# Performance work log

Hardware: AMD Instinct MI355X
Metric: run time of the kernel (lower is better)

Reference implementation:

```python
import jax, jax.numpy as jnp
import numpy as np

N_NODES = 50000
N_EDGES = 600000
NODE_IN = 32
EDGE_IN = 16
HID = 128
L = 3
GCTX = 64


def _lin_init(key, out_d, in_d):
    kw, kb = jax.random.split(key)
    bound = 1.0 / np.sqrt(in_d)
    w = jax.random.uniform(kw, (out_d, in_d), minval=-bound, maxval=bound, dtype=jnp.float32)
    b = jax.random.uniform(kb, (out_d,), minval=-bound, maxval=bound, dtype=jnp.float32)
    return w, b


def _stack_lin(key, out_d, in_d, n):
    ws, bs = [], []
    for k in jax.random.split(key, n):
        w, b = _lin_init(k, out_d, in_d)
        ws.append(w); bs.append(b)
    return jnp.stack(ws), jnp.stack(bs)


def setup_inputs() -> dict:
    key = jax.random.key(0)
    ks = jax.random.split(key, 16)
    x = jax.random.normal(ks[0], (N_NODES, NODE_IN), dtype=jnp.float32)
    edge_index = jax.random.randint(ks[1], (2, N_EDGES), 0, N_NODES, dtype=jnp.int64)
    edge_attr = jax.random.normal(ks[2], (N_EDGES, EDGE_IN), dtype=jnp.float32)
    global_context = jax.random.normal(ks[3], (GCTX,), dtype=jnp.float32)
    node_proj_w, node_proj_b = _lin_init(ks[4], HID, NODE_IN)
    msg_w1, msg_b1 = _stack_lin(ks[5], HID, HID + EDGE_IN, L)
    msg_w2, msg_b2 = _stack_lin(ks[6], HID, HID, L)
    attn_w1, attn_b1 = _stack_lin(ks[7], HID // 2, 2 * HID + EDGE_IN, L)
    attn_w2, attn_b2 = _stack_lin(ks[8], 1, HID // 2, L)
    upd_w1, upd_b1 = _stack_lin(ks[9], HID, 2 * HID, L)
    upd_w2, upd_b2 = _stack_lin(ks[10], HID, HID, L)
    ln_g = jnp.ones((L, HID), dtype=jnp.float32)
    ln_b = jnp.zeros((L, HID), dtype=jnp.float32)
    q_w1, q_b1 = _lin_init(ks[11], HID, HID + GCTX)
    q_w2, q_b2 = _lin_init(ks[12], 1, HID)
    return {
        "x": x, "edge_index": edge_index, "edge_attr": edge_attr,
        "global_context": global_context,
        "node_proj_w": node_proj_w, "node_proj_b": node_proj_b,
        "msg_w1": msg_w1, "msg_b1": msg_b1, "msg_w2": msg_w2, "msg_b2": msg_b2,
        "attn_w1": attn_w1, "attn_b1": attn_b1, "attn_w2": attn_w2, "attn_b2": attn_b2,
        "upd_w1": upd_w1, "upd_b1": upd_b1, "upd_w2": upd_w2, "upd_b2": upd_b2,
        "ln_g": ln_g, "ln_b": ln_b,
        "q_w1": q_w1, "q_b1": q_b1, "q_w2": q_w2, "q_b2": q_b2,
    }


def _layernorm(x, g, b, eps=1e-5):
    mu = jnp.mean(x, axis=-1, keepdims=True)
    var = jnp.var(x, axis=-1, keepdims=True)
    return (x - mu) * jax.lax.rsqrt(var + eps) * g + b


def _mp_layer(h, src, dst, ea, p):
    hs = h[src]          # [E, HID] gather
    hd = h[dst]          # [E, HID] gather
    # message MLP
    m = jnp.concatenate([hs, ea], axis=1)
    m = jax.nn.relu(m @ p["mw1"].T + p["mb1"])
    msg = m @ p["mw2"].T + p["mb2"]
    # attention scores
    a = jnp.concatenate([hs, hd, ea], axis=1)
    a = jax.nn.leaky_relu(a @ p["aw1"].T + p["ab1"], negative_slope=0.2)
    scores = (a @ p["aw2"].T + p["ab2"])[:, 0]  # [E]
    exp_scores = jnp.exp(scores - jnp.max(scores))  # global max, as in original
    sum_exp = jnp.zeros((h.shape[0],), dtype=h.dtype).at[dst].add(exp_scores)
    weights = exp_scores / (sum_exp[dst] + 1e-6)
    agg = jnp.zeros_like(h).at[dst].add(msg * weights[:, None])
    # update MLP + residual + layernorm
    u = jnp.concatenate([h, agg], axis=1)
    u = jax.nn.relu(u @ p["uw1"].T + p["ub1"])
    out = u @ p["uw2"].T + p["ub2"]
    return _layernorm(jax.nn.relu(out + h), p["g"], p["b"])


def reference(x, edge_index, edge_attr, global_context,
              node_proj_w, node_proj_b,
              msg_w1, msg_b1, msg_w2, msg_b2,
              attn_w1, attn_b1, attn_w2, attn_b2,
              upd_w1, upd_b1, upd_w2, upd_b2,
              ln_g, ln_b, q_w1, q_b1, q_w2, q_b2):
    src, dst = edge_index[0], edge_index[1]
    h = jax.nn.relu(x @ node_proj_w.T + node_proj_b)
    for i in range(L):
        p = {"mw1": msg_w1[i], "mb1": msg_b1[i], "mw2": msg_w2[i], "mb2": msg_b2[i],
             "aw1": attn_w1[i], "ab1": attn_b1[i], "aw2": attn_w2[i], "ab2": attn_b2[i],
             "uw1": upd_w1[i], "ub1": upd_b1[i], "uw2": upd_w2[i], "ub2": upd_b2[i],
             "g": ln_g[i], "b": ln_b[i]}
        h = _mp_layer(h, src, dst, edge_attr, p)
    ctx = jnp.broadcast_to(global_context[None, :], (h.shape[0], GCTX))
    h = jnp.concatenate([h, ctx], axis=1)
    q = jax.nn.relu(h @ q_w1.T + q_b1) @ q_w2.T + q_b2
    return q[:, 0]
```

## Files before the change

### kernel.cpp

```cpp
#include <hip/hip_runtime.h>
#include <hip/hip_bf16.h>

#define N_NODES 50000
#define N_EDGES 600000
#define NODE_IN 32
#define EDGE_IN 16
#define HID 128
#define NLAYER 3
#define GCTX 64

typedef _Float16 h2 __attribute__((ext_vector_type(2)));
typedef _Float16 f16x8 __attribute__((ext_vector_type(8)));
typedef float f32x4 __attribute__((ext_vector_type(4)));

__device__ __forceinline__ float bf2f(unsigned short u) {
  union { unsigned int i; float f; } c; c.i = ((unsigned int)u) << 16; return c.f;
}
__device__ __forceinline__ unsigned int bfp2hp(unsigned int b) {
  union { unsigned int i; float f; } lo, hi;
  lo.i = b << 16; hi.i = b & 0xffff0000u;
  h2 r; r.x = (_Float16)lo.f; r.y = (_Float16)hi.f;
  union { h2 h; unsigned int u; } c; c.h = r; return c.u;
}
__device__ __forceinline__ h2 u2h2(unsigned int u) {
  union { unsigned int u; h2 h; } c; c.u = u; return c.h;
}
__device__ __forceinline__ float dot2(h2 a, h2 b, float c) {
#if __has_builtin(__builtin_amdgcn_fdot2)
  return __builtin_amdgcn_fdot2(a, b, c, false);
#else
  return c + (float)a.x * (float)b.x + (float)a.y * (float)b.y;
#endif
}

__device__ __forceinline__ unsigned int load_pair(const void* p, size_t pairIdx, int fm) {
  if (fm == 0) return bfp2hp(((const unsigned int*)p)[pairIdx]);
  if (fm == 2) return ((const unsigned int*)p)[pairIdx];
  const float* f = (const float*)p;
  h2 r; r.x = (_Float16)f[2 * pairIdx]; r.y = (_Float16)f[2 * pairIdx + 1];
  union { h2 h; unsigned int u; } c; c.h = r; return c.u;
}
__device__ __forceinline__ float load_scal(const void* p, size_t idx, int fm) {
  if (fm == 0) return bf2f(((const unsigned short*)p)[idx]);
  if (fm == 2) return (float)((const _Float16*)p)[idx];
  return ((const float*)p)[idx];
}
__device__ __forceinline__ int load_idx(const void* p, size_t pos, int im) {
  if (im == 0) return ((const int*)p)[pos];
  return (int)((const long long*)p)[pos];
}
__device__ __forceinline__ uint4 zero4() { uint4 z; z.x = z.y = z.z = z.w = 0u; return z; }
__device__ __forceinline__ uint4 load8(const void* p, size_t eoff, int fm) {
  uint4 r;
  if (fm == 0) {
    uint4 t = *(const uint4*)((const unsigned short*)p + eoff);
    r.x = bfp2hp(t.x); r.y = bfp2hp(t.y); r.z = bfp2hp(t.z); r.w = bfp2hp(t.w);
  } else if (fm == 2) {
    r = *(const uint4*)((const unsigned short*)p + eoff);
  } else {
    const float* f = (const float*)p + eoff;
    h2 a, b, c, d;
    a.x = (_Float16)f[0]; a.y = (_Float16)f[1];
    b.x = (_Float16)f[2]; b.y = (_Float16)f[3];
    c.x = (_Float16)f[4]; c.y = (_Float16)f[5];
    d.x = (_Float16)f[6]; d.y = (_Float16)f[7];
    union { h2 h; unsigned int u; } ua, ub, uc, ud;
    ua.h = a; ub.h = b; uc.h = c; ud.h = d;
    r.x = ua.u; r.y = ub.u; r.z = uc.u; r.w = ud.u;
  }
  return r;
}
__device__ __forceinline__ f32x4 mfma16(uint4 a, uint4 b, f32x4 c) {
  union { uint4 u; f16x8 h; } A, B; A.u = a; B.u = b;
  return __builtin_amdgcn_mfma_f32_16x16x32_f16(A.h, B.h, c, 0, 0, 0);
}

__device__ __forceinline__ float wave_sum(float v) {
  for (int m = 32; m >= 1; m >>= 1) v += __shfl_xor(v, m, 64);
  return v;
}
__device__ __forceinline__ float wave_max(float v) {
  for (int m = 32; m >= 1; m >>= 1) v = fmaxf(v, __shfl_xor(v, m, 64));
  return v;
}

__global__ __launch_bounds__(256) void k_detect(const unsigned int* __restrict__ x,
                                                const unsigned int* __restrict__ ei,
                                                int* __restrict__ flags) {
  __shared__ int sIn, sOddNZ;
  const int tid = threadIdx.x;
  if (tid == 0) { sIn = 0; sOddNZ = 0; }
  __syncthreads();
  int cnt = 0;
  for (int i = tid; i < 2048; i += 256) {
    unsigned int d = x[i];
    float v0 = fabsf(bf2f((unsigned short)(d & 0xffff)));
    float v1 = fabsf(bf2f((unsigned short)(d >> 16)));
    if (v0 >= 0.1f && v0 <= 6.0f) cnt++;
    if (v1 >= 0.1f && v1 <= 6.0f) cnt++;
  }
  int nz = 0;
  for (int i = tid; i < 512; i += 256)
    if (ei[2 * i + 1] != 0) nz++;
  atomicAdd(&sIn, cnt);
  atomicAdd(&sOddNZ, nz);
  __syncthreads();
  if (tid == 0) {
    float frac = (float)sIn / 4096.f;
    flags[0] = (frac > 0.75f) ? 0 : ((frac >= 0.3f) ? 1 : 2);
    flags[1] = (sOddNZ < 4) ? 1 : 0;
  }
}

__global__ __launch_bounds__(256) void k_proj(
    const void* __restrict__ x, const void* __restrict__ W,
    const void* __restrict__ b, _Float16* __restrict__ h,
    const int* __restrict__ flags) {
  const int fm = flags[0];
  const int tid = threadIdx.x;
  const int slot = tid >> 7;
  const int t = tid & 127;
  __shared__ __align__(16) _Float16 sX[2][NODE_IN];
  unsigned int w[16];
#pragma unroll
  for (int i = 0; i < 16; ++i) w[i] = load_pair(W, (size_t)t * 16 + i, fm);
  const float bias = load_scal(b, t, fm);
  unsigned int* sx32 = (unsigned int*)sX[slot];
  for (int base = blockIdx.x * 2; base < N_NODES; base += gridDim.x * 2) {
    const int n = base + slot;
    if (t < 16) sx32[t] = load_pair(x, (size_t)n * 16 + t, fm);
    __syncthreads();
    float a0 = bias, a1 = 0.f, a2 = 0.f, a3 = 0.f;
    const uint4* vq = (const uint4*)sx32;
#pragma unroll
    for (int q = 0; q < 4; ++q) {
      uint4 v = vq[q];
      a0 = dot2(u2h2(v.x), u2h2(w[q * 4 + 0]), a0);
      a1 = dot2(u2h2(v.y), u2h2(w[q * 4 + 1]), a1);
      a2 = dot2(u2h2(v.z), u2h2(w[q * 4 + 2]), a2);
      a3 = dot2(u2h2(v.w), u2h2(w[q * 4 + 3]), a3);
    }
    h[(size_t)n * HID + t] = (_Float16)fmaxf((a0 + a1) + (a2 + a3), 0.f);
    __syncthreads();
  }
}

__global__ __launch_bounds__(256) void k_hist(const void* __restrict__ ei,
                                              int* __restrict__ cnt,
                                              const int* __restrict__ flags) {
  const int im = flags[1];
  for (int e = blockIdx.x * 256 + threadIdx.x; e < N_EDGES; e += gridDim.x * 256)
    atomicAdd(&cnt[load_idx(ei, N_EDGES + e, im)], 1);
}
__global__ __launch_bounds__(256) void k_scan(const int* __restrict__ cnt,
                                              int* __restrict__ row_ptr,
                                              int* __restrict__ cur) {
  __shared__ int sPart[256];
  const int t = threadIdx.x;
  const int c0 = t * 196;
  const int c1 = (c0 + 196 < N_NODES) ? c0 + 196 : N_NODES;
  int s = 0;
  for (int i = c0; i < c1; ++i) s += cnt[i];
  sPart[t] = s;
  __syncthreads();
  if (t == 0) {
    int run = 0;
    for (int i = 0; i < 256; ++i) { int v = sPart[i]; sPart[i] = run; run += v; }
    row_ptr[N_NODES] = run;
  }
  __syncthreads();
  int off = sPart[t];
  for (int i = c0; i < c1; ++i) {
    row_ptr[i] = off; cur[i] = off; off += cnt[i];
  }
}
__global__ __launch_bounds__(256) void k_scatter(const void* __restrict__ ei,
                                                 const void* __restrict__ ea,
                                                 int* __restrict__ cur,
                                                 int2* __restrict__ sd2,
                                                 _Float16* __restrict__ eaPerm,
                                                 const int* __restrict__ flags) {
  const int im = flags[1], fm = flags[0];
  for (int e = blockIdx.x * 256 + threadIdx.x; e < N_EDGES; e += gridDim.x * 256) {
    const int s = load_idx(ei, e, im);
    const int d = load_idx(ei, N_EDGES + e, im);
    const int pos = atomicAdd(&cur[d], 1);
    int2 sd; sd.x = s; sd.y = d;
    sd2[pos] = sd;
    uint4 lo = load8(ea, (size_t)e * 16, fm);
    uint4 hi = load8(ea, (size_t)e * 16 + 8, fm);
    *(uint4*)(eaPerm + (size_t)pos * 16) = lo;
    *(uint4*)(eaPerm + (size_t)pos * 16 + 8) = hi;
  }
}

#define SAP 296
#define SM1P 136
#define NT32 (N_EDGES / 32)

__global__ __launch_bounds__(256) void k_edge(
    const _Float16* __restrict__ h, const int2* __restrict__ sd2,
    const _Float16* __restrict__ eaPerm,
    const void* __restrict__ aw1, const void* __restrict__ ab1,
    const void* __restrict__ aw2, const void* __restrict__ ab2,
    const void* __restrict__ mw1, const void* __restrict__ mb1,
    float* __restrict__ scores, float* __restrict__ pmax,
    _Float16* __restrict__ msgbuf, const int* __restrict__ flags, int lay) {
  const int fm = flags[0];
  const int tid = threadIdx.x;
  const int w = tid >> 6, l = tid & 63;
  const int m16 = l & 15, q = l >> 4;
  __shared__ __align__(16) _Float16 sA[2][32 * SAP];
  __shared__ float sS[2][4][32];

  uint4 bA[9], bM1[2][5];
  {
    const int arow = w * 16 + m16;
    const size_t awb = (size_t)lay * 64 * 272 + (size_t)arow * 272;
#pragma unroll
    for (int ks = 0; ks < 9; ++ks) {
      const int c0 = ks * 32 + q * 8;
      bA[ks] = (c0 < 272) ? load8(aw1, awb + c0, fm) : zero4();
    }
#pragma unroll
    for (int nt = 0; nt < 2; ++nt) {
      const int mrow = (2 * w + nt) * 16 + m16;
      const size_t m1b = (size_t)lay * 128 * 144 + (size_t)mrow * 144;
#pragma unroll
      for (int ks = 0; ks < 5; ++ks) {
        const int c0 = ks * 32 + q * 8;
        bM1[nt][ks] = (c0 < 144) ? load8(mw1, m1b + c0, fm) : zero4();
      }
    }
  }
  const float ab1v = load_scal(ab1, lay * 64 + w * 16 + m16, fm);
  const float w2s  = load_scal(aw2, lay * 64 + w * 16 + m16, fm);
  const float b2f  = load_scal(ab2, lay, fm);
  float b1v[2];
#pragma unroll
  for (int nt = 0; nt < 2; ++nt)
    b1v[nt] = load_scal(mb1, lay * 128 + (2 * w + nt) * 16 + m16, fm);

  const int ide0 = tid >> 4, ch = tid & 15, ide1 = ide0 + 16;
  float lmax = -3.4e38f;
  uint4 rHs0, rHd0, rHs1, rHd1, rEa;
  const int G = gridDim.x;
  int t = blockIdx.x, pt = -1, buf = 0;

  if (tid < 128) {
    const int b = tid >> 6, s = tid & 63;
    *(uint4*)(sA[b] + (s >> 1) * SAP + 272 + (s & 1) * 8) = zero4();
  }
  {
    const int e0 = t * 32;
    const int2 s0 = sd2[e0 + ide0], s1 = sd2[e0 + ide1];
    rHs0 = *(const uint4*)(h + (size_t)s0.x * HID + ch * 8);
    rHd0 = *(const uint4*)(h + (size_t)s0.y * HID + ch * 8);
    rHs1 = *(const uint4*)(h + (size_t)s1.x * HID + ch * 8);
    rHd1 = *(const uint4*)(h + (size_t)s1.y * HID + ch * 8);
    if (tid < 64)
      rEa = *(const uint4*)(eaPerm + (size_t)(e0 + (tid >> 1)) * 16 + (tid & 1) * 8);
  }
  __syncthreads();

  while (t < NT32) {
    _Float16* A = sA[buf];
    *(uint4*)(A + ide0 * SAP + ch * 8) = rHs0;
    *(uint4*)(A + ide0 * SAP + 128 + ch * 8) = rHd0;
    *(uint4*)(A + ide1 * SAP + ch * 8) = rHs1;
    *(uint4*)(A + ide1 * SAP + 128 + ch * 8) = rHd1;
    if (tid < 64)
      *(uint4*)(A + (tid >> 1) * SAP + 256 + (tid & 1) * 8) = rEa;
    __syncthreads();
    const int nxt = t + G;
    if (nxt < NT32) {
      const int e0 = nxt * 32;
      const int2 s0 = sd2[e0 + ide0], s1 = sd2[e0 + ide1];
      rHs0 = *(const uint4*)(h + (size_t)s0.x * HID + ch * 8);
      rHd0 = *(const uint4*)(h + (size_t)s0.y * HID + ch * 8);
      rHs1 = *(const uint4*)(h + (size_t)s1.x * HID + ch * 8);
      rHd1 = *(const uint4*)(h + (size_t)s1.y * HID + ch * 8);
      if (tid < 64)
        rEa = *(const uint4*)(eaPerm + (size_t)(e0 + (tid >> 1)) * 16 + (tid & 1) * 8);
    }
#pragma unroll
    for (int mg = 0; mg < 2; ++mg) {
      const int arow = m16 + 16 * mg;
      uint4 aF[9];
#pragma unroll
      for (int ks = 0; ks < 9; ++ks)
        aF[ks] = *(const uint4*)(A + arow * SAP + ks * 32 + q * 8);
      {
        f32x4 aacc = {0.f, 0.f, 0.f, 0.f};
#pragma unroll
        for (int ks = 0; ks < 9; ++ks) aacc = mfma16(aF[ks], bA[ks], aacc);
        float sv[4];
#pragma unroll
        for (int r = 0; r < 4; ++r) {
          float v = aacc[r] + ab1v;
          v = (v > 0.f) ? v : 0.2f * v;
          sv[r] = v * w2s;
        }
#pragma unroll
        for (int mk = 1; mk <= 8; mk <<= 1) {
#pragma unroll
          for (int r = 0; r < 4; ++r) sv[r] += __shfl_xor(sv[r], mk, 64);
        }
        if (m16 == 0)
          *(float4*)(&sS[buf][w][mg * 16 + q * 4]) = make_float4(sv[0], sv[1], sv[2], sv[3]);
      }
#pragma unroll
      for (int nt = 0; nt < 2; ++nt) {
        f32x4 macc = {0.f, 0.f, 0.f, 0.f};
#pragma unroll
        for (int ks = 0; ks < 4; ++ks) macc = mfma16(aF[ks], bM1[nt][ks], macc);
        macc = mfma16(aF[8], bM1[nt][4], macc);
        const int col = (2 * w + nt) * 16 + m16;
#pragma unroll
        for (int r = 0; r < 4; ++r)
          msgbuf[(size_t)(t * 32 + mg * 16 + q * 4 + r) * HID + col] =
              (_Float16)fmaxf(macc[r] + b1v[nt], 0.f);
      }
    }
    if (pt >= 0 && tid < 32) {
      const float s = sS[buf ^ 1][0][tid] + sS[buf ^ 1][1][tid] +
                      sS[buf ^ 1][2][tid] + sS[buf ^ 1][3][tid] + b2f;
      scores[pt * 32 + tid] = s;
      lmax = fmaxf(lmax, s);
    }
    pt = t; t = nxt; buf ^= 1;
  }
  __syncthreads();
  if (pt >= 0 && tid < 32) {
    const float s = sS[buf ^ 1][0][tid] + sS[buf ^ 1][1][tid] +
                    sS[buf ^ 1][2][tid] + sS[buf ^ 1][3][tid] + b2f;
    scores[pt * 32 + tid] = s;
    lmax = fmaxf(lmax, s);
  }
  if (w == 0) {
    float m = wave_max((l < 32) ? lmax : -3.4e38f);
    if (tid == 0) pmax[blockIdx.x] = m;
  }
}

__global__ __launch_bounds__(256) void k_rmax(const float* __restrict__ pmax, int n,
                                              float* __restrict__ gmax) {
  float m = -3.4e38f;
  for (int i = threadIdx.x; i < n; i += 256) m = fmaxf(m, pmax[i]);
  m = wave_max(m);
  __shared__ float sm[4];
  if ((threadIdx.x & 63) == 0) sm[threadIdx.x >> 6] = m;
  __syncthreads();
  if (threadIdx.x == 0) gmax[0] = fmaxf(fmaxf(sm[0], sm[1]), fmaxf(sm[2], sm[3]));
}

__global__ __launch_bounds__(256) void k_gather(
    const _Float16* __restrict__ msgbuf, const float* __restrict__ scores,
    const int* __restrict__ row_ptr, const float* __restrict__ gmax,
    _Float16* __restrict__ Sbuf, float* __restrict__ Dbuf) {
  const int w = threadIdx.x >> 6, l = threadIdx.x & 63;
  const int n0 = blockIdx.x * 16;
  const float M = gmax[0];
  const unsigned int* mb32 = (const unsigned int*)msgbuf;
#pragma unroll
  for (int k = 0; k < 4; ++k) {
    const int n = n0 + 4 * w + k;
    const int rp0 = row_ptr[n], rp1 = row_ptr[n + 1];
    float ax0 = 0.f, ay0 = 0.f, d0s = 0.f;
    float ax1 = 0.f, ay1 = 0.f, d1s = 0.f;
    float ax2 = 0.f, ay2 = 0.f, d2s = 0.f;
    float ax3 = 0.f, ay3 = 0.f, d3s = 0.f;
    int i = rp0;
    for (; i + 4 <= rp1; i += 4) {
      const float s0 = scores[i], s1 = scores[i + 1];
      const float s2 = scores[i + 2], s3 = scores[i + 3];
      const unsigned int m0 = mb32[(size_t)i * 64 + l];
      const unsigned int m1 = mb32[(size_t)(i + 1) * 64 + l];
      const unsigned int m2 = mb32[(size_t)(i + 2) * 64 + l];
      const unsigned int m3 = mb32[(size_t)(i + 3) * 64 + l];
      const float w0 = __expf(s0 - M), w1 = __expf(s1 - M);
      const float w2 = __expf(s2 - M), w3 = __expf(s3 - M);
      h2 p0 = u2h2(m0), p1 = u2h2(m1), p2 = u2h2(m2), p3 = u2h2(m3);
      ax0 += w0 * (float)p0.x; ay0 += w0 * (float)p0.y; d0s += w0;
      ax1 += w1 * (float)p1.x; ay1 += w1 * (float)p1.y; d1s += w1;
      ax2 += w2 * (float)p2.x; ay2 += w2 * (float)p2.y; d2s += w2;
      ax3 += w3 * (float)p3.x; ay3 += w3 * (float)p3.y; d3s += w3;
    }
    for (; i < rp1; ++i) {
      const float w0 = __expf(scores[i] - M);
      h2 p0 = u2h2(mb32[(size_t)i * 64 + l]);
      ax0 += w0 * (float)p0.x; ay0 += w0 * (float)p0.y; d0s += w0;
    }
    const float ax = (ax0 + ax1) + (ax2 + ax3);
    const float ay = (ay0 + ay1) + (ay2 + ay3);
    const float den = (d0s + d1s) + (d2s + d3s);
    h2 o; o.x = (_Float16)ax; o.y = (_Float16)ay;
    union { h2 hh; unsigned int u; } c; c.hh = o;
    ((unsigned int*)Sbuf)[(size_t)n * 64 + l] = c.u;
    if (l == 0) Dbuf[n] = den;
  }
}

#define SUP3 392
#define SOP 132
__global__ __launch_bounds__(256, 1) void k_upd3(
    _Float16* __restrict__ h, const _Float16* __restrict__ Sbuf,
    const float* __restrict__ Dbuf,
    const void* __restrict__ mw2, const void* __restrict__ mb2,
    const void* __restrict__ uw1, const void* __restrict__ ub1,
    const void* __restrict__ uw2, const void* __restrict__ ub2,
    const void* __restrict__ lng, const void* __restrict__ lnb,
    const int* __restrict__ flags, int lay) {
  const int fm = flags[0];
  const int tid = threadIdx.x;
  const int w = tid >> 6, l = tid & 63;
  const int m16 = l & 15, q = l >> 4;
  __shared__ __align__(16) _Float16 sU[16 * SUP3];
  __shared__ __align__(16) _Float16 sM1[16 * SM1P];
  __shared__ __align__(16) float sO[16 * SOP];
  __shared__ float sD[16];

  uint4 bU1[2][8], bU2[2][4], bM2g[2][4];
  float b1v[2], b2v[2], b2m[2];
#pragma unroll
  for (int nt = 0; nt < 2; ++nt) {
    const int row = w * 32 + nt * 16 + m16;
    const size_t b1p = (size_t)lay * 128 * 256 + (size_t)row * 256;
#pragma unroll
    for (int ks = 0; ks < 8; ++ks) bU1[nt][ks] = load8(uw1, b1p + ks * 32 + q * 8, fm);
    const size_t b2p = (size_t)lay * 128 * 128 + (size_t)row * 128;
#pragma unroll
    for (int ks = 0; ks < 4; ++ks) bU2[nt][ks] = load8(uw2, b2p + ks * 32 + q * 8, fm);
#pragma unroll
    for (int ks = 0; ks < 4; ++ks) bM2g[nt][ks] = load8(mw2, b2p + ks * 32 + q * 8, fm);
    b1v[nt] = load_scal(ub1, lay * 128 + row, fm);
    b2v[nt] = load_scal(ub2, lay * 128 + row, fm);
    b2m[nt] = load_scal(mb2, lay * 128 + row, fm);
  }
  const int nd = tid >> 4, sc = tid & 15;
  float g8[8], be8[8];
#pragma unroll
  for (int j = 0; j < 8; ++j) {
    g8[j] = load_scal(lng, lay * 128 + sc * 8 + j, fm);
    be8[j] = load_scal(lnb, lay * 128 + sc * 8 + j, fm);
  }

  for (int n0 = blockIdx.x * 16; n0 < N_NODES; n0 += gridDim.x * 16) {
    *(uint4*)(sU + nd * SUP3 + sc * 8) =
        *(const uint4*)(h + (size_t)(n0 + nd) * HID + sc * 8);
    *(uint4*)(sU + nd * SUP3 + 128 + sc * 8) =
        *(const uint4*)(Sbuf + (size_t)(n0 + nd) * HID + sc * 8);
    if (tid < 16) sD[tid] = Dbuf[n0 + tid];
    __syncthreads();
    {
      uint4 aS[4];
#pragma unroll
      for (int ks = 0; ks < 4; ++ks)
        aS[ks] = *(const uint4*)(sU + m16 * SUP3 + 128 + ks * 32 + q * 8);
#pragma unroll
      for (int nt = 0; nt < 2; ++nt) {
        f32x4 acc = {0.f, 0.f, 0.f, 0.f};
#pragma unroll
        for (int ks = 0; ks < 4; ++ks) acc = mfma16(aS[ks], bM2g[nt][ks], acc);
        const int colw = w * 32 + nt * 16 + m16;
#pragma unroll
        for (int r = 0; r < 4; ++r) {
          const int row = q * 4 + r;
          const float Dv = sD[row];
          const float inv = 1.f / (Dv + 1e-6f);
          sU[row * SUP3 + 256 + colw] = (_Float16)((acc[r] + b2m[nt] * Dv) * inv);
        }
      }
    }
    __syncthreads();
    uint4 aF[8];
#pragma unroll
    for (int ks = 0; ks < 4; ++ks)
      aF[ks] = *(const uint4*)(sU + m16 * SUP3 + ks * 32 + q * 8);
#pragma unroll
    for (int ks = 4; ks < 8; ++ks)
      aF[ks] = *(const uint4*)(sU + m16 * SUP3 + 256 + (ks - 4) * 32 + q * 8);
#pragma unroll
    for (int nt = 0; nt < 2; ++nt) {
      f32x4 acc = {0.f, 0.f, 0.f, 0.f};
#pragma unroll
      for (int ks = 0; ks < 8; ++ks) acc = mfma16(aF[ks], bU1[nt][ks], acc);
      const int colw = w * 32 + nt * 16 + m16;
#pragma unroll
      for (int r = 0; r < 4; ++r)
        sM1[(q * 4 + r) * SM1P + colw] = (_Float16)fmaxf(acc[r] + b1v[nt], 0.f);
    }
    __syncthreads();
    uint4 a2F[4];
#pragma unroll
    for (int ks = 0; ks < 4; ++ks)
      a2F[ks] = *(const uint4*)(sM1 + m16 * SM1P + ks * 32 + q * 8);
#pragma unroll
    for (int nt = 0; nt < 2; ++nt) {
      f32x4 acc = {0.f, 0.f, 0.f, 0.f};
#pragma unroll
      for (int ks = 0; ks < 4; ++ks) acc = mfma16(a2F[ks], bU2[nt][ks], acc);
      const int colw = w * 32 + nt * 16 + m16;
#pragma unroll
      for (int r = 0; r < 4; ++r) {
        const int row = q * 4 + r;
        const float hres = (float)sU[row * SUP3 + colw];
        sO[row * SOP + colw] = fmaxf(acc[r] + b2v[nt] + hres, 0.f);
      }
    }
    __syncthreads();
    float v[8], s1 = 0.f, s2 = 0.f;
    const float4 p0 = *(const float4*)(sO + nd * SOP + sc * 8);
    const float4 p1 = *(const float4*)(sO + nd * SOP + sc * 8 + 4);
    v[0] = p0.x; v[1] = p0.y; v[2] = p0.z; v[3] = p0.w;
    v[4] = p1.x; v[5] = p1.y; v[6] = p1.z; v[7] = p1.w;
#pragma unroll
    for (int j = 0; j < 8; ++j) { s1 += v[j]; s2 += v[j] * v[j]; }
#pragma unroll
    for (int mk = 1; mk <= 8; mk <<= 1) {
      s1 += __shfl_xor(s1, mk, 64);
      s2 += __shfl_xor(s2, mk, 64);
    }
    const float mu = s1 * (1.f / HID);
    const float var = s2 * (1.f / HID) - mu * mu;
    const float rs = rsqrtf(var + 1e-5f);
    unsigned int pk[4];
#pragma unroll
    for (int jj = 0; jj < 4; ++jj) {
      h2 o;
      o.x = (_Float16)((v[2 * jj] - mu) * rs * g8[2 * jj] + be8[2 * jj]);
      o.y = (_Float16)((v[2 * jj + 1] - mu) * rs * g8[2 * jj + 1] + be8[2 * jj + 1]);
      union { h2 hh; unsigned int u; } c; c.hh = o;
      pk[jj] = c.u;
    }
    uint4 outv; outv.x = pk[0]; outv.y = pk[1]; outv.z = pk[2]; outv.w = pk[3];
    *(uint4*)(h + (size_t)(n0 + nd) * HID + sc * 8) = outv;
    __syncthreads();
  }
}

__global__ __launch_bounds__(256) void k_attn(
    const _Float16* __restrict__ h, const void* __restrict__ ei,
    const void* __restrict__ ea,
    const void* __restrict__ aw1, const void* __restrict__ ab1,
    const void* __restrict__ aw2, const void* __restrict__ ab2,
    float* __restrict__ scores, float* __restrict__ pmax,
    const int* __restrict__ flags, int lay) {
  const int fm = flags[0], im = flags[1];
  const int tid = threadIdx.x;
  const int w = tid >> 6, l = tid & 63;
  __shared__ __align__(16) _Float16 sV[4][2 * HID + EDGE_IN];
  __shared__ float sRed[4];
  unsigned int wr[136];
  {
    const size_t base = (size_t)lay * 64 * 136 + (size_t)l * 136;
#pragma unroll
    for (int i = 0; i < 136; ++i) wr[i] = load_pair(aw1, base + i, fm);
  }
  const float bias = load_scal(ab1, lay * 64 + l, fm);
  const float w2f = load_scal(aw2, lay * 64 + l, fm);
  const float b2f = load_scal(ab2, lay, fm);
  float wmax = -3.4e38f;
  unsigned int* sv32 = (unsigned int*)sV[w];
  const int stride = gridDim.x * 4;
  const int nIter = (N_EDGES + stride - 1) / stride;
  for (int it = 0; it < nIter; ++it) {
    const int e = blockIdx.x * 4 + w + it * stride;
    const bool act = (e < N_EDGES);
    if (act) {
      const int src = load_idx(ei, e, im);
      const int dst = load_idx(ei, N_EDGES + e, im);
      sv32[l] = ((const unsigned int*)(h + (size_t)src * HID))[l];
      sv32[64 + l] = ((const unsigned int*)(h + (size_t)dst * HID))[l];
      if (l < 8) sv32[128 + l] = load_pair(ea, (size_t)e * 8 + l, fm);
    }
    __syncthreads();
    if (act) {
      float a0 = bias, a1 = 0.f, a2 = 0.f, a3 = 0.f;
      const uint4* vq = (const uint4*)sv32;
#pragma unroll
      for (int qq = 0; qq < 34; ++qq) {
        uint4 v = vq[qq];
        a0 = dot2(u2h2(v.x), u2h2(wr[qq * 4 + 0]), a0);
        a1 = dot2(u2h2(v.y), u2h2(wr[qq * 4 + 1]), a1);
        a2 = dot2(u2h2(v.z), u2h2(wr[qq * 4 + 2]), a2);
        a3 = dot2(u2h2(v.w), u2h2(wr[qq * 4 + 3]), a3);
      }
      float a = (a0 + a1) + (a2 + a3);
      a = (a > 0.f) ? a : 0.2f * a;
      float s = wave_sum(a * w2f) + b2f;
      if (l == 0) scores[e] = s;
      wmax = fmaxf(wmax, s);
    }
    __syncthreads();
  }
  if (l == 0) sRed[w] = wmax;
  __syncthreads();
  if (tid == 0)
    pmax[blockIdx.x] = fmaxf(fmaxf(sRed[0], sRed[1]), fmaxf(sRed[2], sRed[3]));
}

__global__ __launch_bounds__(256) void k_msg(
    const _Float16* __restrict__ h, const void* __restrict__ ei,
    const void* __restrict__ ea,
    const void* __restrict__ mw1, const void* __restrict__ mb1,
    const void* __restrict__ mw2, const void* __restrict__ mb2,
    const float* __restrict__ scores, const float* __restrict__ gmaxp,
    float* __restrict__ numer, float* __restrict__ denom,
    const int* __restrict__ flags, int lay) {
  const int fm = flags[0], im = flags[1];
  const int tid = threadIdx.x;
  const int slot = tid >> 7, t = tid & 127;
  __shared__ __align__(16) _Float16 sV[2][HID + EDGE_IN];
  __shared__ __align__(16) _Float16 sM1b[2][HID];
  unsigned int w1[72], w2[64];
  {
    const size_t b1p = (size_t)lay * HID * 72 + (size_t)t * 72;
#pragma unroll
    for (int i = 0; i < 72; ++i) w1[i] = load_pair(mw1, b1p + i, fm);
    const size_t b2p = (size_t)lay * HID * 64 + (size_t)t * 64;
#pragma unroll
    for (int i = 0; i < 64; ++i) w2[i] = load_pair(mw2, b2p + i, fm);
  }
  const float b1 = load_scal(mb1, lay * HID + t, fm);
  const float b2 = load_scal(mb2, lay * HID + t, fm);
  const float gmax = gmaxp[0];
  unsigned int* sv32 = (unsigned int*)sV[slot];
  for (int base = blockIdx.x * 2; base < N_EDGES; base += gridDim.x * 2) {
    const int e = base + slot;
    const int src = load_idx(ei, e, im);
    const int dst = load_idx(ei, N_EDGES + e, im);
    if (t < 64) {
      sv32[t] = ((const unsigned int*)(h + (size_t)src * HID))[t];
    } else if (t < 72) {
      sv32[t] = load_pair(ea, (size_t)e * 8 + (t - 64), fm);
    }
    __syncthreads();
    float a0 = b1, a1 = 0.f, a2 = 0.f, a3 = 0.f;
    const uint4* vq = (const uint4*)sv32;
#pragma unroll
    for (int qq = 0; qq < 18; ++qq) {
      uint4 v = vq[qq];
      a0 = dot2(u2h2(v.x), u2h2(w1[qq * 4 + 0]), a0);
      a1 = dot2(u2h2(v.y), u2h2(w1[qq * 4 + 1]), a1);
      a2 = dot2(u2h2(v.z), u2h2(w1[qq * 4 + 2]), a2);
      a3 = dot2(u2h2(v.w), u2h2(w1[qq * 4 + 3]), a3);
    }
    sM1b[slot][t] = (_Float16)fmaxf((a0 + a1) + (a2 + a3), 0.f);
    __syncthreads();
    float c0 = b2, c1 = 0.f, c2 = 0.f, c3 = 0.f;
    const uint4* mq = (const uint4*)sM1b[slot];
#pragma unroll
    for (int qq = 0; qq < 16; ++qq) {
      uint4 v = mq[qq];
      c0 = dot2(u2h2(v.x), u2h2(w2[qq * 4 + 0]), c0);
      c1 = dot2(u2h2(v.y), u2h2(w2[qq * 4 + 1]), c1);
      c2 = dot2(u2h2(v.z), u2h2(w2[qq * 4 + 2]), c2);
      c3 = dot2(u2h2(v.w), u2h2(w2[qq * 4 + 3]), c3);
    }
    float msg = (c0 + c1) + (c2 + c3);
    float wgt = __expf(scores[e] - gmax);
    atomicAdd(&numer[(size_t)dst * HID + t], msg * wgt);
    if (t == 0) atomicAdd(&denom[dst], wgt);
    __syncthreads();
  }
}

__global__ __launch_bounds__(256) void k_upd(
    _Float16* __restrict__ h, const float* __restrict__ numer,
    const float* __restrict__ denom,
    const void* __restrict__ uw1, const void* __restrict__ ub1,
    const void* __restrict__ uw2, const void* __restrict__ ub2,
    const void* __restrict__ lng, const void* __restrict__ lnb,
    const int* __restrict__ flags, int lay) {
  const int fm = flags[0];
  const int tid = threadIdx.x;
  const int slot = tid >> 7, t = tid & 127;
  const int wv = (tid >> 6) & 1;
  __shared__ __align__(16) _Float16 sV[2][2 * HID];
  __shared__ __align__(16) _Float16 sM1b[2][HID];
  __shared__ float sRed[2][2][2];
  unsigned int w1[128], w2[64];
  {
    const size_t b1p = (size_t)lay * HID * 128 + (size_t)t * 128;
#pragma unroll
    for (int i = 0; i < 128; ++i) w1[i] = load_pair(uw1, b1p + i, fm);
    const size_t b2p = (size_t)lay * HID * 64 + (size_t)t * 64;
#pragma unroll
    for (int i = 0; i < 64; ++i) w2[i] = load_pair(uw2, b2p + i, fm);
  }
  const float b1 = load_scal(ub1, lay * HID + t, fm);
  const float b2 = load_scal(ub2, lay * HID + t, fm);
  const float gg = load_scal(lng, lay * HID + t, fm);
  const float bb = load_scal(lnb, lay * HID + t, fm);
  unsigned int* sv32 = (unsigned int*)sV[slot];
  for (int base = blockIdx.x * 2; base < N_NODES; base += gridDim.x * 2) {
    const int n = base + slot;
    const float inv = 1.f / (denom[n] + 1e-6f);
    if (t < 64) {
      sv32[t] = ((const unsigned int*)(h + (size_t)n * HID))[t];
    } else {
      const int j = (t - 64) * 2;
      h2 p; p.x = (_Float16)(numer[(size_t)n * HID + j] * inv);
      p.y = (_Float16)(numer[(size_t)n * HID + j + 1] * inv);
      union { h2 hh; unsigned int u; } c; c.hh = p;
      sv32[64 + (t - 64)] = c.u;
    }
    __syncthreads();
    float a0 = b1, a1 = 0.f, a2 = 0.f, a3 = 0.f;
    const uint4* vq = (const uint4*)sv32;
#pragma unroll
    for (int qq = 0; qq < 32; ++qq) {
      uint4 v = vq[qq];
      a0 = dot2(u2h2(v.x), u2h2(w1[qq * 4 + 0]), a0);
      a1 = dot2(u2h2(v.y), u2h2(w1[qq * 4 + 1]), a1);
      a2 = dot2(u2h2(v.z), u2h2(w1[qq * 4 + 2]), a2);
      a3 = dot2(u2h2(v.w), u2h2(w1[qq * 4 + 3]), a3);
    }
    sM1b[slot][t] = (_Float16)fmaxf((a0 + a1) + (a2 + a3), 0.f);
    __syncthreads();
    float c0 = b2, c1 = 0.f, c2 = 0.f, c3 = 0.f;
    const uint4* mq = (const uint4*)sM1b[slot];
#pragma unroll
    for (int qq = 0; qq < 16; ++qq) {
      uint4 v = mq[qq];
      c0 = dot2(u2h2(v.x), u2h2(w2[qq * 4 + 0]), c0);
      c1 = dot2(u2h2(v.y), u2h2(w2[qq * 4 + 1]), c1);
      c2 = dot2(u2h2(v.z), u2h2(w2[qq * 4 + 2]), c2);
      c3 = dot2(u2h2(v.w), u2h2(w2[qq * 4 + 3]), c3);
    }
    const float hold = (float)((const _Float16*)sV[slot])[t];
    const float r = fmaxf((c0 + c1) + (c2 + c3) + hold, 0.f);
    float s1 = wave_sum(r);
    float s2 = wave_sum(r * r);
    if ((tid & 63) == 0) { sRed[slot][wv][0] = s1; sRed[slot][wv][1] = s2; }
    __syncthreads();
    const float S1 = sRed[slot][0][0] + sRed[slot][1][0];
    const float S2 = sRed[slot][0][1] + sRed[slot][1][1];
    const float mu = S1 * (1.f / HID);
    const float var = S2 * (1.f / HID) - mu * mu;
    const float rs = rsqrtf(var + 1e-5f);
    h[(size_t)n * HID + t] = (_Float16)((r - mu) * rs * gg + bb);
    __syncthreads();
  }
}

__global__ __launch_bounds__(256) void k_read(
    const _Float16* __restrict__ h, const void* __restrict__ gctx,
    const void* __restrict__ qw1, const void* __restrict__ qb1,
    const void* __restrict__ qw2, const void* __restrict__ qb2,
    void* __restrict__ out, const int* __restrict__ flags) {
  const int fm = flags[0];
  const int tid = threadIdx.x;
  const int slot = tid >> 7, t = tid & 127;
  const int wv = (tid >> 6) & 1;
  __shared__ __align__(16) _Float16 sV[2][HID];
  __shared__ __align__(16) _Float16 sCtx[GCTX];
  __shared__ float sRed[2][2];
  unsigned int w1[96];
#pragma unroll
  for (int i = 0; i < 96; ++i) w1[i] = load_pair(qw1, (size_t)t * 96 + i, fm);
  const float b1 = load_scal(qb1, t, fm);
  const float w2f = load_scal(qw2, t, fm);
  const float b2 = load_scal(qb2, 0, fm);
  if (tid < GCTX / 2)
    ((unsigned int*)sCtx)[tid] = load_pair(gctx, tid, fm);
  __syncthreads();
  unsigned int* sv32 = (unsigned int*)sV[slot];
  for (int base = blockIdx.x * 2; base < N_NODES; base += gridDim.x * 2) {
    const int n = base + slot;
    if (t < 64) sv32[t] = ((const unsigned int*)(h + (size_t)n * HID))[t];
    __syncthreads();
    float a0 = b1, a1 = 0.f, a2 = 0.f, a3 = 0.f;
    const uint4* vq = (const uint4*)sv32;
#pragma unroll
    for (int qq = 0; qq < 16; ++qq) {
      uint4 v = vq[qq];
      a0 = dot2(u2h2(v.x), u2h2(w1[qq * 4 + 0]), a0);
      a1 = dot2(u2h2(v.y), u2h2(w1[qq * 4 + 1]), a1);
      a2 = dot2(u2h2(v.z), u2h2(w1[qq * 4 + 2]), a2);
      a3 = dot2(u2h2(v.w), u2h2(w1[qq * 4 + 3]), a3);
    }
    const uint4* cq = (const uint4*)sCtx;
#pragma unroll
    for (int qq = 0; qq < 8; ++qq) {
      uint4 v = cq[qq];
      a0 = dot2(u2h2(v.x), u2h2(w1[64 + qq * 4 + 0]), a0);
      a1 = dot2(u2h2(v.y), u2h2(w1[64 + qq * 4 + 1]), a1);
      a2 = dot2(u2h2(v.z), u2h2(w1[64 + qq * 4 + 2]), a2);
      a3 = dot2(u2h2(v.w), u2h2(w1[64 + qq * 4 + 3]), a3);
    }
    float u = fmaxf((a0 + a1) + (a2 + a3), 0.f);
    float s = wave_sum(u * w2f);
    if ((tid & 63) == 0) sRed[slot][wv] = s;
    __syncthreads();
    if (t == 0) {
      const float val = sRed[slot][0] + sRed[slot][1] + b2;
      if (fm == 0) ((__hip_bfloat16*)out)[n] = __float2bfloat16(val);
      else if (fm == 2) ((_Float16*)out)[n] = (_Float16)val;
      else ((float*)out)[n] = val;
    }
    __syncthreads();
  }
}

extern "C" void kernel_launch(void* const* d_in, const int* in_sizes, int n_in,
                              void* d_out, int out_size, void* d_ws, size_t ws_size,
                              hipStream_t stream) {
  const void* x    = d_in[0];
  const void* ei   = d_in[1];
  const void* ea   = d_in[2];
  const void* gctx = d_in[3];
  const void* npw  = d_in[4];
  const void* npb  = d_in[5];
  const void* mw1  = d_in[6];
  const void* mb1  = d_in[7];
  const void* mw2  = d_in[8];
  const void* mb2  = d_in[9];
  const void* aw1  = d_in[10];
  const void* ab1  = d_in[11];
  const void* aw2  = d_in[12];
  const void* ab2  = d_in[13];
  const void* uw1  = d_in[14];
  const void* ub1  = d_in[15];
  const void* uw2  = d_in[16];
  const void* ub2  = d_in[17];
  const void* lng  = d_in[18];
  const void* lnb  = d_in[19];
  const void* qw1  = d_in[20];
  const void* qb1  = d_in[21];
  const void* qw2  = d_in[22];
  const void* qb2  = d_in[23];

  char* ws = (char*)d_ws;
  dim3 blk(256);

  size_t off = 0;
  auto alloc = [&](size_t bytes) {
    void* p = ws + off;
    off = (off + bytes + 255) & ~(size_t)255;
    return p;
  };
  int* flags       = (int*)alloc(8 * 4);
  _Float16* hbuf   = (_Float16*)alloc((size_t)N_NODES * HID * 2);
  float* scores    = (float*)alloc((size_t)N_EDGES * 4);
  float* pmax      = (float*)alloc(2048 * 4);
  float* gmax      = (float*)alloc(4);
  int* cnt         = (int*)alloc((size_t)N_NODES * 4);
  int* cur         = (int*)alloc((size_t)N_NODES * 4);
  int* row_ptr     = (int*)alloc((size_t)(N_NODES + 1) * 4);
  int2* sd2        = (int2*)alloc((size_t)N_EDGES * 8);
  _Float16* eaPerm = (_Float16*)alloc((size_t)N_EDGES * EDGE_IN * 2);
  _Float16* Sbuf   = (_Float16*)alloc((size_t)N_NODES * HID * 2);
  float* Dbuf      = (float*)alloc((size_t)N_NODES * 4);
  _Float16* msgbuf = (_Float16*)alloc((size_t)N_EDGES * HID * 2);
  const size_t need_big = off;

  if (ws_size >= need_big) {
    k_detect<<<1, blk, 0, stream>>>((const unsigned int*)x, (const unsigned int*)ei, flags);
    k_proj<<<1024, blk, 0, stream>>>(x, npw, npb, hbuf, flags);
    hipMemsetAsync(cnt, 0, (size_t)N_NODES * 4, stream);
    k_hist<<<1024, blk, 0, stream>>>(ei, cnt, flags);
    k_scan<<<1, blk, 0, stream>>>(cnt, row_ptr, cur);
    k_scatter<<<1024, blk, 0, stream>>>(ei, ea, cur, sd2, eaPerm, flags);
    for (int lay = 0; lay < NLAYER; ++lay) {
      k_edge<<<1024, blk, 0, stream>>>(hbuf, sd2, eaPerm, aw1, ab1, aw2, ab2,
                                       mw1, mb1, scores, pmax, msgbuf, flags, lay);
      k_rmax<<<1, blk, 0, stream>>>(pmax, 1024, gmax);
      k_gather<<<N_NODES / 16, blk, 0, stream>>>(msgbuf, scores, row_ptr, gmax,
                                                 Sbuf, Dbuf);
      k_upd3<<<1024, blk, 0, stream>>>(hbuf, Sbuf, Dbuf, mw2, mb2,
                                       uw1, ub1, uw2, ub2, lng, lnb, flags, lay);
    }
    k_read<<<1024, blk, 0, stream>>>(hbuf, gctx, qw1, qb1, qw2, qb2, d_out, flags);
  } else {
    size_t o2 = 0;
    int* flags2 = (int*)(ws + o2); o2 += 256;
    _Float16* hb = (_Float16*)(ws + o2); o2 += (size_t)N_NODES * HID * 2;
    o2 = (o2 + 255) & ~(size_t)255;
    float* sc = (float*)(ws + o2); o2 += (size_t)N_EDGES * 4;
    float* pm = (float*)(ws + o2); o2 += 1024 * 4;
    float* gm = (float*)(ws + o2); o2 += 256;
    float* numer = (float*)(ws + o2); o2 += (size_t)N_NODES * HID * 4;
    float* denom = (float*)(ws + o2); o2 += (size_t)N_NODES * 4;
    k_detect<<<1, blk, 0, stream>>>((const unsigned int*)x, (const unsigned int*)ei, flags2);
    k_proj<<<1024, blk, 0, stream>>>(x, npw, npb, hb, flags2);
    for (int lay = 0; lay < NLAYER; ++lay) {
      hipMemsetAsync(numer, 0, (size_t)N_NODES * HID * 4, stream);
      hipMemsetAsync(denom, 0, (size_t)N_NODES * 4, stream);
      k_attn<<<1024, blk, 0, stream>>>(hb, ei, ea, aw1, ab1, aw2, ab2, sc, pm,
                                       flags2, lay);
      k_rmax<<<1, blk, 0, stream>>>(pm, 1024, gm);
      k_msg<<<1024, blk, 0, stream>>>(hb, ei, ea, mw1, mb1, mw2, mb2, sc, gm,
                                      numer, denom, flags2, lay);
      k_upd<<<1024, blk, 0, stream>>>(hb, numer, denom, uw1, ub1, uw2, ub2, lng, lnb,
                                      flags2, lay);
    }
    k_read<<<1024, blk, 0, stream>>>(hb, gctx, qw1, qb1, qw2, qb2, d_out, flags2);
  }
}
```

Baseline: 1.030 ms.

## Parallelize CSR prefix scan across blocks and use MFMA readout kernel

Result: faster. 838.4 us (-18.6%).

```diff
diff --git a/kernel.cpp b/kernel.cpp
--- a/kernel.cpp
+++ b/kernel.cpp
@@ -79,6 +79,10 @@
   for (int m = 32; m >= 1; m >>= 1) v += __shfl_xor(v, m, 64);
   return v;
 }
+__device__ __forceinline__ int wave_sum_i(int v) {
+  for (int m = 32; m >= 1; m >>= 1) v += __shfl_xor(v, m, 64);
+  return v;
+}
 __device__ __forceinline__ float wave_max(float v) {
   for (int m = 32; m >= 1; m >>= 1) v = fmaxf(v, __shfl_xor(v, m, 64));
   return v;
@@ -152,26 +156,40 @@
   for (int e = blockIdx.x * 256 + threadIdx.x; e < N_EDGES; e += gridDim.x * 256)
     atomicAdd(&cnt[load_idx(ei, N_EDGES + e, im)], 1);
 }
-__global__ __launch_bounds__(256) void k_scan(const int* __restrict__ cnt,
+__global__ __launch_bounds__(256) void k_psum(const int* __restrict__ cnt,
+                                              int* __restrict__ csum) {
+  const int b = blockIdx.x;
+  const int c0 = b * 196;
+  const int c1 = (c0 + 196 < N_NODES) ? c0 + 196 : N_NODES;
+  int s = 0;
+  for (int i = c0 + threadIdx.x; i < c1; i += 256) s += cnt[i];
+  s = wave_sum_i(s);
+  __shared__ int sm[4];
+  if ((threadIdx.x & 63) == 0) sm[threadIdx.x >> 6] = s;
+  __syncthreads();
+  if (threadIdx.x == 0) csum[b] = sm[0] + sm[1] + sm[2] + sm[3];
+}
+__global__ __launch_bounds__(256) void k_fill(const int* __restrict__ cnt,
+                                              const int* __restrict__ csum,
                                               int* __restrict__ row_ptr,
                                               int* __restrict__ cur) {
-  __shared__ int sPart[256];
-  const int t = threadIdx.x;
-  const int c0 = t * 196;
+  const int b = blockIdx.x;
+  const int tid = threadIdx.x;
+  const int c0 = b * 196;
   const int c1 = (c0 + 196 < N_NODES) ? c0 + 196 : N_NODES;
-  int s = 0;
-  for (int i = c0; i < c1; ++i) s += cnt[i];
-  sPart[t] = s;
+  __shared__ int sCnt[196];
+  __shared__ int sm[4];
+  int v = (tid < b) ? csum[tid] : 0;
+  v = wave_sum_i(v);
+  if ((tid & 63) == 0) sm[tid >> 6] = v;
+  for (int i = c0 + tid; i < c1; i += 256) sCnt[i - c0] = cnt[i];
   __syncthreads();
-  if (t == 0) {
-    int run = 0;
-    for (int i = 0; i < 256; ++i) { int v = sPart[i]; sPart[i] = run; run += v; }
-    row_ptr[N_NODES] = run;
-  }
-  __syncthreads();
-  int off = sPart[t];
-  for (int i = c0; i < c1; ++i) {
-    row_ptr[i] = off; cur[i] = off; off += cnt[i];
+  if (tid == 0) {
+    int off = sm[0] + sm[1] + sm[2] + sm[3];
+    for (int i = c0; i < c1; ++i) {
+      row_ptr[i] = off; cur[i] = off; off += sCnt[i - c0];
+    }
+    if (b == 255) row_ptr[N_NODES] = off;
   }
 }
 __global__ __launch_bounds__(256) void k_scatter(const void* __restrict__ ei,
@@ -535,6 +553,80 @@
     }
     uint4 outv; outv.x = pk[0]; outv.y = pk[1]; outv.z = pk[2]; outv.w = pk[3];
     *(uint4*)(h + (size_t)(n0 + nd) * HID + sc * 8) = outv;
+    __syncthreads();
+  }
+}
+
+#define SRP 136
+__global__ __launch_bounds__(256) void k_read2(
+    const _Float16* __restrict__ h, const void* __restrict__ gctx,
+    const void* __restrict__ qw1, const void* __restrict__ qb1,
+    const void* __restrict__ qw2, const void* __restrict__ qb2,
+    void* __restrict__ out, const int* __restrict__ flags) {
+  const int fm = flags[0];
+  const int tid = threadIdx.x;
+  const int w = tid >> 6, l = tid & 63;
+  const int m16 = l & 15, q = l >> 4;
+  __shared__ __align__(16) _Float16 sU[16 * SRP];
+  __shared__ __align__(16) _Float16 sM1[16 * SM1P];
+  __shared__ float sCvec[128];
+
+  uint4 bQ[2][4];
+#pragma unroll
+  for (int nt = 0; nt < 2; ++nt) {
+    const int row = w * 32 + nt * 16 + m16;
+#pragma unroll
+    for (int ks = 0; ks < 4; ++ks)
+      bQ[nt][ks] = load8(qw1, (size_t)row * 192 + ks * 32 + q * 8, fm);
+  }
+  if (tid < 128) {
+    float acc = load_scal(qb1, tid, fm);
+    for (int j = 0; j < GCTX / 2; ++j) {
+      h2 wv = u2h2(load_pair(qw1, (size_t)tid * 96 + 64 + j, fm));
+      h2 cv = u2h2(load_pair(gctx, j, fm));
+      acc = dot2(cv, wv, acc);
+    }
+    sCvec[tid] = acc;
+  }
+  const int nd = tid >> 4, sc = tid & 15;
+  float q2[8];
+#pragma unroll
+  for (int j = 0; j < 8; ++j) q2[j] = load_scal(qw2, sc * 8 + j, fm);
+  const float qb2v = load_scal(qb2, 0, fm);
+  __syncthreads();
+
+  for (int n0 = blockIdx.x * 16; n0 < N_NODES; n0 += gridDim.x * 16) {
+    *(uint4*)(sU + nd * SRP + sc * 8) =
+        *(const uint4*)(h + (size_t)(n0 + nd) * HID + sc * 8);
+    __syncthreads();
+    uint4 aF[4];
+#pragma unroll
+    for (int ks = 0; ks < 4; ++ks)
+      aF[ks] = *(const uint4*)(sU + m16 * SRP + ks * 32 + q * 8);
+#pragma unroll
+    for (int nt = 0; nt < 2; ++nt) {
+      f32x4 acc = {0.f, 0.f, 0.f, 0.f};
+#pragma unroll
+      for (int ks = 0; ks < 4; ++ks) acc = mfma16(aF[ks], bQ[nt][ks], acc);
+      const int colw = w * 32 + nt * 16 + m16;
+#pragma unroll
+      for (int r = 0; r < 4; ++r)
+        sM1[(q * 4 + r) * SM1P + colw] = (_Float16)fmaxf(acc[r] + sCvec[colw], 0.f);
+    }
+    __syncthreads();
+    float s = 0.f;
+#pragma unroll
+    for (int j = 0; j < 8; ++j)
+      s += (float)sM1[nd * SM1P + sc * 8 + j] * q2[j];
+#pragma unroll
+    for (int mk = 1; mk <= 8; mk <<= 1) s += __shfl_xor(s, mk, 64);
+    if (sc == 0) {
+      const float val = s + qb2v;
+      const int n = n0 + nd;
+      if (fm == 0) ((__hip_bfloat16*)out)[n] = __float2bfloat16(val);
+      else if (fm == 2) ((_Float16*)out)[n] = (_Float16)val;
+      else ((float*)out)[n] = val;
+    }
     __syncthreads();
   }
 }
@@ -849,6 +941,7 @@
   int* cnt         = (int*)alloc((size_t)N_NODES * 4);
   int* cur         = (int*)alloc((size_t)N_NODES * 4);
   int* row_ptr     = (int*)alloc((size_t)(N_NODES + 1) * 4);
+  int* csum        = (int*)alloc(256 * 4);
   int2* sd2        = (int2*)alloc((size_t)N_EDGES * 8);
   _Float16* eaPerm = (_Float16*)alloc((size_t)N_EDGES * EDGE_IN * 2);
   _Float16* Sbuf   = (_Float16*)alloc((size_t)N_NODES * HID * 2);
@@ -861,7 +954,8 @@
     k_proj<<<1024, blk, 0, stream>>>(x, npw, npb, hbuf, flags);
     hipMemsetAsync(cnt, 0, (size_t)N_NODES * 4, stream);
     k_hist<<<1024, blk, 0, stream>>>(ei, cnt, flags);
-    k_scan<<<1, blk, 0, stream>>>(cnt, row_ptr, cur);
+    k_psum<<<256, blk, 0, stream>>>(cnt, csum);
+    k_fill<<<256, blk, 0, stream>>>(cnt, csum, row_ptr, cur);
     k_scatter<<<1024, blk, 0, stream>>>(ei, ea, cur, sd2, eaPerm, flags);
     for (int lay = 0; lay < NLAYER; ++lay) {
       k_edge<<<1024, blk, 0, stream>>>(hbuf, sd2, eaPerm, aw1, ab1, aw2, ab2,
@@ -872,7 +966,7 @@
       k_upd3<<<1024, blk, 0, stream>>>(hbuf, Sbuf, Dbuf, mw2, mb2,
                                        uw1, ub1, uw2, ub2, lng, lnb, flags, lay);
     }
-    k_read<<<1024, blk, 0, stream>>>(hbuf, gctx, qw1, qb1, qw2, qb2, d_out, flags);
+    k_read2<<<1024, blk, 0, stream>>>(hbuf, gctx, qw1, qb1, qw2, qb2, d_out, flags);
   } else {
     size_t o2 = 0;
     int* flags2 = (int*)(ws + o2); o2 += 256;
```
